# Kernel optimization log

Measured on AMD Instinct MI355X. Metric: run time of the kernel, lower is better.

The kernel has to match this reference:

```python
import jax, jax.numpy as jnp
import numpy as np

# UDH_UPPER-style 16-joint upper-body skeleton tree (edge list in topological order)
N = 16
PARENT = [0, 1, 2, 3, 4, 3, 6, 7, 8, 9, 3, 11, 12, 13, 14]
CHILD = [1, 2, 3, 4, 5, 6, 7, 8, 9, 10, 11, 12, 13, 14, 15]
BATCH = 262144


def rotation_6d_to_matrix(d6):
    """Zhou et al. 6d -> 3x3 rotation. d6: [..., 6] -> [..., 3, 3] (rows b1,b2,b3)."""
    a1, a2 = d6[..., :3], d6[..., 3:]
    b1 = a1 / jnp.linalg.norm(a1, axis=-1, keepdims=True)
    b2 = a2 - jnp.sum(b1 * a2, axis=-1, keepdims=True) * b1
    b2 = b2 / jnp.linalg.norm(b2, axis=-1, keepdims=True)
    b3 = jnp.cross(b1, b2)
    return jnp.stack((b1, b2, b3), axis=-2)


def setup_inputs() -> dict:
    key = jax.random.key(0)
    k1, k2 = jax.random.split(key)
    angles = jax.random.normal(k1, (BATCH, N, 6), dtype=jnp.float32)
    # reference skeleton landmark positions (buffer self.xyz), shape [1, N, 3]
    xyz = jax.random.normal(k2, (1, N, 3), dtype=jnp.float32)
    return {"angles": angles, "xyz": xyz}


def reference(angles, xyz):
    """Skeleton.points: 6d angles -> world-space joint XYZ, shape [B, N, 3].

    Faithful to _rotation2points: M[c] = M[p] @ m(rot_c, xyz_c - xyz_p),
    where m packs (r, r @ t) into a rigid transform; we track the rigid
    transform as (R_world [B,3,3], p_world [B,3]) instead of 4x4 matrices.
    """
    R = rotation_6d_to_matrix(angles)  # [B, N, 3, 3]
    ref = xyz[0]                       # [N, 3]
    Rw = [None] * N
    pw = [None] * N
    # root: M[0] = m(rot[:,0], xyz[:,0])
    Rw[0] = R[:, 0]
    pw[0] = jnp.einsum('bij,j->bi', R[:, 0], ref[0])
    for p, c in zip(PARENT, CHILD):
        t = ref[c] - ref[p]                              # [3] bone offset
        local_t = jnp.einsum('bij,j->bi', R[:, c], t)    # r @ t
        Rw[c] = jnp.einsum('bij,bjk->bik', Rw[p], R[:, c])
        pw[c] = jnp.einsum('bij,bj->bi', Rw[p], local_t) + pw[p]
    return jnp.stack(pw, axis=1)  # [B, N, 3] == stack(M)[..., :3, 3]
```

## Files before the change

kernel.cpp:

```cpp
#include <hip/hip_runtime.h>


namespace {

constexpr int NJ = 16;

__device__ __forceinline__ void rot6d(const float* __restrict__ a, float R[9]) {
    float inv1 = rsqrtf(a[0]*a[0] + a[1]*a[1] + a[2]*a[2]);
    float b10 = a[0]*inv1, b11 = a[1]*inv1, b12 = a[2]*inv1;
    float d = b10*a[3] + b11*a[4] + b12*a[5];
    float c0 = a[3] - d*b10, c1 = a[4] - d*b11, c2 = a[5] - d*b12;
    float inv2 = rsqrtf(c0*c0 + c1*c1 + c2*c2);
    float b20 = c0*inv2, b21 = c1*inv2, b22 = c2*inv2;
    R[0] = b10; R[1] = b11; R[2] = b12;
    R[3] = b20; R[4] = b21; R[5] = b22;
    R[6] = b11*b22 - b12*b21;
    R[7] = b12*b20 - b10*b22;
    R[8] = b10*b21 - b11*b20;
}

__global__ __launch_bounds__(256) void skel_kernel(
    const float* __restrict__ angles,
    const float* __restrict__ xyz,
    float* __restrict__ out,
    int batch)
{
    const int b = blockIdx.x * 256 + threadIdx.x;
    if (b >= batch) return;

    const float4* a4 = (const float4*)(angles + (size_t)b * (NJ * 6));
    float af[NJ * 6];
#pragma unroll
    for (int k = 0; k < 24; ++k) {
        float4 v = a4[k];
        af[4*k + 0] = v.x; af[4*k + 1] = v.y; af[4*k + 2] = v.z; af[4*k + 3] = v.w;
    }

    float* ob = out + (size_t)b * (NJ * 3);

    float R[9], Rw[9], pw[3], Rw3[9], pw3[3];

    rot6d(&af[0], Rw);
    {
        float x = xyz[0], y = xyz[1], z = xyz[2];
        pw[0] = Rw[0]*x + Rw[1]*y + Rw[2]*z;
        pw[1] = Rw[3]*x + Rw[4]*y + Rw[5]*z;
        pw[2] = Rw[6]*x + Rw[7]*y + Rw[8]*z;
    }
    ob[0] = pw[0]; ob[1] = pw[1]; ob[2] = pw[2];

    constexpr int PAR[15] = {0, 1, 2, 3, 4, 3, 6, 7, 8, 9, 3, 11, 12, 13, 14};

#pragma unroll
    for (int e = 0; e < 15; ++e) {
        const int c = e + 1;
        const int p = PAR[e];

        if (p == 3) {
#pragma unroll
            for (int k = 0; k < 9; ++k) Rw[k] = Rw3[k];
            pw[0] = pw3[0]; pw[1] = pw3[1]; pw[2] = pw3[2];
        }

        rot6d(&af[c * 6], R);

        float tx = xyz[c * 3 + 0] - xyz[p * 3 + 0];
        float ty = xyz[c * 3 + 1] - xyz[p * 3 + 1];
        float tz = xyz[c * 3 + 2] - xyz[p * 3 + 2];

        float lt0 = R[0]*tx + R[1]*ty + R[2]*tz;
        float lt1 = R[3]*tx + R[4]*ty + R[5]*tz;
        float lt2 = R[6]*tx + R[7]*ty + R[8]*tz;

        float np0 = Rw[0]*lt0 + Rw[1]*lt1 + Rw[2]*lt2 + pw[0];
        float np1 = Rw[3]*lt0 + Rw[4]*lt1 + Rw[5]*lt2 + pw[1];
        float np2 = Rw[6]*lt0 + Rw[7]*lt1 + Rw[8]*lt2 + pw[2];

        float T[9];
#pragma unroll
        for (int i = 0; i < 3; ++i)
#pragma unroll
            for (int j = 0; j < 3; ++j)
                T[i*3 + j] = Rw[i*3 + 0]*R[0*3 + j]
                           + Rw[i*3 + 1]*R[1*3 + j]
                           + Rw[i*3 + 2]*R[2*3 + j];
#pragma unroll
        for (int k = 0; k < 9; ++k) Rw[k] = T[k];
        pw[0] = np0; pw[1] = np1; pw[2] = np2;

        ob[c*3 + 0] = np0; ob[c*3 + 1] = np1; ob[c*3 + 2] = np2;

        if (c == 3) {
#pragma unroll
            for (int k = 0; k < 9; ++k) Rw3[k] = Rw[k];
            pw3[0] = pw[0]; pw3[1] = pw[1]; pw3[2] = pw[2];
        }
    }
}

}

extern "C" void kernel_launch(void* const* d_in, const int* in_sizes, int n_in,
                              void* d_out, int out_size, void* d_ws, size_t ws_size,
                              hipStream_t stream) {
    const float* angles = (const float*)d_in[0];
    const float* xyz    = (const float*)d_in[1];
    float* out          = (float*)d_out;

    const int batch = in_sizes[0] / (NJ * 6);
    dim3 grid((batch + 255) / 256);
    skel_kernel<<<grid, 256, 0, stream>>>(angles, xyz, out, batch);
}
```

Before: 203.9 us.

## Stage angle loads and output stores through LDS for coalesced wave access

Each wave now cooperatively loads four joints' angles for its 64 elements into a padded LDS tile, so the global reads are contiguous, then each lane reads back its own values. Outputs are written the same way, transposed through LDS and emitted as coalesced float4 stores. Before, each thread read and wrote a strided 384-byte and 192-byte record. The kinematic chain is split into four passes to keep register pressure low, and launch bounds request 4 blocks per CU. This adds many __syncthreads and LDS traffic in exchange for better global memory coalescing.

```diff
diff --git a/kernel.cpp b/kernel.cpp
--- a/kernel.cpp
+++ b/kernel.cpp
@@ -19,83 +19,178 @@
     R[8] = b10*b21 - b11*b20;
 }
 
-__global__ __launch_bounds__(256) void skel_kernel(
+__device__ __forceinline__ void chain_step(const float R[9],
+                                           float tx, float ty, float tz,
+                                           float Rw[9], float pw[3]) {
+    float lt0 = R[0]*tx + R[1]*ty + R[2]*tz;
+    float lt1 = R[3]*tx + R[4]*ty + R[5]*tz;
+    float lt2 = R[6]*tx + R[7]*ty + R[8]*tz;
+    float np0 = Rw[0]*lt0 + Rw[1]*lt1 + Rw[2]*lt2 + pw[0];
+    float np1 = Rw[3]*lt0 + Rw[4]*lt1 + Rw[5]*lt2 + pw[1];
+    float np2 = Rw[6]*lt0 + Rw[7]*lt1 + Rw[8]*lt2 + pw[2];
+    float T[9];
+#pragma unroll
+    for (int i = 0; i < 3; ++i)
+#pragma unroll
+        for (int j = 0; j < 3; ++j)
+            T[i*3 + j] = Rw[i*3 + 0]*R[0*3 + j]
+                       + Rw[i*3 + 1]*R[1*3 + j]
+                       + Rw[i*3 + 2]*R[2*3 + j];
+#pragma unroll
+    for (int k = 0; k < 9; ++k) Rw[k] = T[k];
+    pw[0] = np0; pw[1] = np1; pw[2] = np2;
+}
+
+__global__ __launch_bounds__(256, 4) void skel_kernel(
     const float* __restrict__ angles,
     const float* __restrict__ xyz,
     float* __restrict__ out,
     int batch)
 {
-    const int b = blockIdx.x * 256 + threadIdx.x;
-    if (b >= batch) return;
-
-    const float4* a4 = (const float4*)(angles + (size_t)b * (NJ * 6));
-    float af[NJ * 6];
-#pragma unroll
-    for (int k = 0; k < 24; ++k) {
-        float4 v = a4[k];
-        af[4*k + 0] = v.x; af[4*k + 1] = v.y; af[4*k + 2] = v.z; af[4*k + 3] = v.w;
-    }
-
-    float* ob = out + (size_t)b * (NJ * 3);
-
-    float R[9], Rw[9], pw[3], Rw3[9], pw3[3];
-
-    rot6d(&af[0], Rw);
+    __shared__ float4 lds[4 * 64 * 7];
+
+    const int tid  = threadIdx.x;
+    const int wave = tid >> 6;
+    const int lane = tid & 63;
+    float4* W = &lds[wave * (64 * 7)];
+
+    const int waveElem = blockIdx.x * 256 + wave * 64;
+    const int myElem   = waveElem + lane;
+    const bool meOk    = (myElem < batch);
+
+    const float4* ang4 = (const float4*)angles;
+    float4*       out4 = (float4*)out;
+
+    auto load_pass = [&](int p) {
+#pragma unroll
+        for (int j = 0; j < 6; ++j) {
+            int flat = 64 * j + lane;
+            int le = flat / 6;
+            int lc = flat - 6 * le;
+            int ge = waveElem + le;
+            float4 v = make_float4(0.f, 0.f, 0.f, 0.f);
+            if (ge < batch) v = ang4[(size_t)ge * 24 + p * 6 + lc];
+            W[le * 7 + lc] = v;
+        }
+    };
+
+    auto read_mine = [&](float* a) {
+#pragma unroll
+        for (int c = 0; c < 6; ++c) {
+            float4 v = W[lane * 7 + c];
+            a[4*c + 0] = v.x; a[4*c + 1] = v.y; a[4*c + 2] = v.z; a[4*c + 3] = v.w;
+        }
+    };
+
+    auto store_pass = [&](int p, const float* o) {
+        W[lane * 7 + 0] = make_float4(o[0], o[1], o[2],  o[3]);
+        W[lane * 7 + 1] = make_float4(o[4], o[5], o[6],  o[7]);
+        W[lane * 7 + 2] = make_float4(o[8], o[9], o[10], o[11]);
+        __syncthreads();
+#pragma unroll
+        for (int j = 0; j < 3; ++j) {
+            int flat = 64 * j + lane;
+            int le = flat / 3;
+            int lc = flat - 3 * le;
+            int ge = waveElem + le;
+            if (ge < batch) out4[(size_t)ge * 12 + p * 3 + lc] = W[le * 7 + lc];
+        }
+    };
+
+    auto tvec = [&](int c, int p, float& tx, float& ty, float& tz) {
+        tx = xyz[c*3 + 0] - xyz[p*3 + 0];
+        ty = xyz[c*3 + 1] - xyz[p*3 + 1];
+        tz = xyz[c*3 + 2] - xyz[p*3 + 2];
+    };
+
+    float Rw[9], pw[3], Rw3[9], pw3[3];
+    float a[24], R[9], o[12];
+    float tx, ty, tz;
+
+    load_pass(0);
+    __syncthreads();
+    read_mine(a);
+
+    rot6d(&a[0], Rw);
     {
         float x = xyz[0], y = xyz[1], z = xyz[2];
         pw[0] = Rw[0]*x + Rw[1]*y + Rw[2]*z;
         pw[1] = Rw[3]*x + Rw[4]*y + Rw[5]*z;
         pw[2] = Rw[6]*x + Rw[7]*y + Rw[8]*z;
     }
-    ob[0] = pw[0]; ob[1] = pw[1]; ob[2] = pw[2];
-
-    constexpr int PAR[15] = {0, 1, 2, 3, 4, 3, 6, 7, 8, 9, 3, 11, 12, 13, 14};
-
-#pragma unroll
-    for (int e = 0; e < 15; ++e) {
-        const int c = e + 1;
-        const int p = PAR[e];
-
-        if (p == 3) {
-#pragma unroll
-            for (int k = 0; k < 9; ++k) Rw[k] = Rw3[k];
-            pw[0] = pw3[0]; pw[1] = pw3[1]; pw[2] = pw3[2];
-        }
-
-        rot6d(&af[c * 6], R);
-
-        float tx = xyz[c * 3 + 0] - xyz[p * 3 + 0];
-        float ty = xyz[c * 3 + 1] - xyz[p * 3 + 1];
-        float tz = xyz[c * 3 + 2] - xyz[p * 3 + 2];
-
-        float lt0 = R[0]*tx + R[1]*ty + R[2]*tz;
-        float lt1 = R[3]*tx + R[4]*ty + R[5]*tz;
-        float lt2 = R[6]*tx + R[7]*ty + R[8]*tz;
-
-        float np0 = Rw[0]*lt0 + Rw[1]*lt1 + Rw[2]*lt2 + pw[0];
-        float np1 = Rw[3]*lt0 + Rw[4]*lt1 + Rw[5]*lt2 + pw[1];
-        float np2 = Rw[6]*lt0 + Rw[7]*lt1 + Rw[8]*lt2 + pw[2];
-
-        float T[9];
-#pragma unroll
-        for (int i = 0; i < 3; ++i)
-#pragma unroll
-            for (int j = 0; j < 3; ++j)
-                T[i*3 + j] = Rw[i*3 + 0]*R[0*3 + j]
-                           + Rw[i*3 + 1]*R[1*3 + j]
-                           + Rw[i*3 + 2]*R[2*3 + j];
-#pragma unroll
-        for (int k = 0; k < 9; ++k) Rw[k] = T[k];
-        pw[0] = np0; pw[1] = np1; pw[2] = np2;
-
-        ob[c*3 + 0] = np0; ob[c*3 + 1] = np1; ob[c*3 + 2] = np2;
-
-        if (c == 3) {
-#pragma unroll
-            for (int k = 0; k < 9; ++k) Rw3[k] = Rw[k];
-            pw3[0] = pw[0]; pw3[1] = pw[1]; pw3[2] = pw[2];
-        }
-    }
+    o[0] = pw[0]; o[1] = pw[1]; o[2] = pw[2];
+
+    rot6d(&a[6], R);  tvec(1, 0, tx, ty, tz); chain_step(R, tx, ty, tz, Rw, pw);
+    o[3] = pw[0]; o[4] = pw[1]; o[5] = pw[2];
+    rot6d(&a[12], R); tvec(2, 1, tx, ty, tz); chain_step(R, tx, ty, tz, Rw, pw);
+    o[6] = pw[0]; o[7] = pw[1]; o[8] = pw[2];
+    rot6d(&a[18], R); tvec(3, 2, tx, ty, tz); chain_step(R, tx, ty, tz, Rw, pw);
+    o[9] = pw[0]; o[10] = pw[1]; o[11] = pw[2];
+
+#pragma unroll
+    for (int k = 0; k < 9; ++k) Rw3[k] = Rw[k];
+    pw3[0] = pw[0]; pw3[1] = pw[1]; pw3[2] = pw[2];
+
+    store_pass(0, o);
+    __syncthreads();
+
+    load_pass(1);
+    __syncthreads();
+    read_mine(a);
+
+    rot6d(&a[0], R);  tvec(4, 3, tx, ty, tz); chain_step(R, tx, ty, tz, Rw, pw);
+    o[0] = pw[0]; o[1] = pw[1]; o[2] = pw[2];
+    rot6d(&a[6], R);  tvec(5, 4, tx, ty, tz); chain_step(R, tx, ty, tz, Rw, pw);
+    o[3] = pw[0]; o[4] = pw[1]; o[5] = pw[2];
+
+#pragma unroll
+    for (int k = 0; k < 9; ++k) Rw[k] = Rw3[k];
+    pw[0] = pw3[0]; pw[1] = pw3[1]; pw[2] = pw3[2];
+
+    rot6d(&a[12], R); tvec(6, 3, tx, ty, tz); chain_step(R, tx, ty, tz, Rw, pw);
+    o[6] = pw[0]; o[7] = pw[1]; o[8] = pw[2];
+    rot6d(&a[18], R); tvec(7, 6, tx, ty, tz); chain_step(R, tx, ty, tz, Rw, pw);
+    o[9] = pw[0]; o[10] = pw[1]; o[11] = pw[2];
+
+    store_pass(1, o);
+    __syncthreads();
+
+    load_pass(2);
+    __syncthreads();
+    read_mine(a);
+
+    rot6d(&a[0], R);  tvec(8, 7, tx, ty, tz); chain_step(R, tx, ty, tz, Rw, pw);
+    o[0] = pw[0]; o[1] = pw[1]; o[2] = pw[2];
+    rot6d(&a[6], R);  tvec(9, 8, tx, ty, tz); chain_step(R, tx, ty, tz, Rw, pw);
+    o[3] = pw[0]; o[4] = pw[1]; o[5] = pw[2];
+    rot6d(&a[12], R); tvec(10, 9, tx, ty, tz); chain_step(R, tx, ty, tz, Rw, pw);
+    o[6] = pw[0]; o[7] = pw[1]; o[8] = pw[2];
+
+#pragma unroll
+    for (int k = 0; k < 9; ++k) Rw[k] = Rw3[k];
+    pw[0] = pw3[0]; pw[1] = pw3[1]; pw[2] = pw3[2];
+
+    rot6d(&a[18], R); tvec(11, 3, tx, ty, tz); chain_step(R, tx, ty, tz, Rw, pw);
+    o[9] = pw[0]; o[10] = pw[1]; o[11] = pw[2];
+
+    store_pass(2, o);
+    __syncthreads();
+
+    load_pass(3);
+    __syncthreads();
+    read_mine(a);
+
+    rot6d(&a[0], R);  tvec(12, 11, tx, ty, tz); chain_step(R, tx, ty, tz, Rw, pw);
+    o[0] = pw[0]; o[1] = pw[1]; o[2] = pw[2];
+    rot6d(&a[6], R);  tvec(13, 12, tx, ty, tz); chain_step(R, tx, ty, tz, Rw, pw);
+    o[3] = pw[0]; o[4] = pw[1]; o[5] = pw[2];
+    rot6d(&a[12], R); tvec(14, 13, tx, ty, tz); chain_step(R, tx, ty, tz, Rw, pw);
+    o[6] = pw[0]; o[7] = pw[1]; o[8] = pw[2];
+    rot6d(&a[18], R); tvec(15, 14, tx, ty, tz); chain_step(R, tx, ty, tz, Rw, pw);
+    o[9] = pw[0]; o[10] = pw[1]; o[11] = pw[2];
+
+    store_pass(3, o);
+    (void)meOk;
 }
 
 }
```

Measured after the change: 217.5 us. 1.07x slower.
